# Kernel tuning notes

Measured on AMD Instinct MI355X. Metric: run time of the kernel, lower is better.

The kernel has to match this reference:

```python
import jax, jax.numpy as jnp
import numpy as np

EPS_BN = 1e-5
EPS_W = 1e-8


def _bn(x, g, b, m, v):
    # x: [B, N, C]; params: [C] (inference-mode batchnorm)
    return g * (x - m) * jax.lax.rsqrt(v + EPS_BN) + b


def setup_inputs() -> dict:
    key = jax.random.key(0)
    ks = jax.random.split(key, 24)
    B, N, S = 16, 4096, 1024
    C1, C2 = 128, 256            # points1 / points2 channels
    CIN, COUT = C1 + C2, 128     # in_channel, out_channel

    def w(k, shape, std=0.02):
        return (jax.random.normal(k, shape, jnp.float32) * std)

    def bn_params(k, c):
        k1, k2, k3, k4 = jax.random.split(k, 4)
        return (1.0 + 0.1 * jax.random.normal(k1, (c,), jnp.float32),  # gamma
                0.1 * jax.random.normal(k2, (c,), jnp.float32),        # beta
                0.1 * jax.random.normal(k3, (c,), jnp.float32),        # running mean
                0.5 + jax.random.uniform(k4, (c,), jnp.float32))       # running var

    fg, fb, fm, fv = bn_params(ks[4], COUT)
    g1, b1, m1, v1 = bn_params(ks[5], COUT)
    g2, b2, m2, v2 = bn_params(ks[6], COUT)
    return {
        "xyz1": jax.random.uniform(ks[0], (B, N, 3), jnp.float32),
        "xyz2": jax.random.uniform(ks[1], (B, S, 3), jnp.float32),
        "points1": jax.random.normal(ks[2], (B, C1, N), jnp.float32),
        "points2": jax.random.normal(ks[3], (B, C2, S), jnp.float32),
        "fuse_w": w(ks[7], (COUT, CIN)), "fuse_b": jnp.zeros((COUT,), jnp.float32),
        "fuse_g": fg, "fuse_beta": fb, "fuse_m": fm, "fuse_v": fv,
        "c1_w": w(ks[8], (COUT, COUT)), "c1_b": jnp.zeros((COUT,), jnp.float32),
        "bn1_g": g1, "bn1_b": b1, "bn1_m": m1, "bn1_v": v1,
        "c2_w": w(ks[9], (COUT, COUT)), "c2_b": jnp.zeros((COUT,), jnp.float32),
        "bn2_g": g2, "bn2_b": b2, "bn2_m": m2, "bn2_v": v2,
    }


def reference(xyz1, xyz2, points1, points2,
              fuse_w, fuse_b, fuse_g, fuse_beta, fuse_m, fuse_v,
              c1_w, c1_b, bn1_g, bn1_b, bn1_m, bn1_v,
              c2_w, c2_b, bn2_g, bn2_b, bn2_m, bn2_v):
    B, N, _ = xyz1.shape
    pts1 = jnp.swapaxes(points1, 1, 2)   # [B, N, C1]
    pts2 = jnp.swapaxes(points2, 1, 2)   # [B, S, C2]

    # squared pairwise distances [B, N, S]
    dists = (jnp.sum(xyz1 ** 2, -1)[:, :, None]
             + jnp.sum(xyz2 ** 2, -1)[:, None, :]
             - 2.0 * jnp.einsum('bnc,bsc->bns', xyz1, xyz2))

    # 3 nearest neighbors (smallest distances)
    neg_d3, idx = jax.lax.top_k(-dists, 3)          # [B, N, 3]
    d3 = -neg_d3
    recip = 1.0 / (d3 + EPS_W)
    weight = recip / jnp.sum(recip, axis=2, keepdims=True)  # [B, N, 3]

    gathered = jax.vmap(lambda p, i: p[i])(pts2, idx)        # [B, N, 3, C2]
    interp = jnp.sum(gathered * weight[..., None], axis=2)   # [B, N, C2]

    x = jnp.concatenate([pts1, interp], axis=-1)             # [B, N, CIN]

    # fuse: 1x1 conv + BN + ReLU
    x = jax.nn.relu(_bn(jnp.einsum('bnc,oc->bno', x, fuse_w) + fuse_b,
                        fuse_g, fuse_beta, fuse_m, fuse_v))

    # residual block: conv-BN-ReLU -> conv-BN, add skip, ReLU
    h = jax.nn.relu(_bn(jnp.einsum('bnc,oc->bno', x, c1_w) + c1_b,
                        bn1_g, bn1_b, bn1_m, bn1_v))
    y = _bn(jnp.einsum('bnc,oc->bno', h, c2_w) + c2_b,
            bn2_g, bn2_b, bn2_m, bn2_v)
    out = jax.nn.relu(y + x)                                 # [B, N, COUT]
    return jnp.swapaxes(out, 1, 2)                           # [B, COUT, N]
```

## Files before the change

kernel.cpp:

```cpp
#include <hip/hip_runtime.h>
#include <hip/hip_bf16.h>

#define BB 16
#define NN 4096
#define SS 1024
#define C1 128
#define C2 256
#define CIN 384
#define CO 128

#define KCH 8
#define SCH (SS / KCH)

typedef __bf16 bf16x8 __attribute__((ext_vector_type(8)));
typedef float f32x4 __attribute__((ext_vector_type(4)));

__global__ __launch_bounds__(256) void knn_part_kernel(
    const float* __restrict__ xyz1, const float* __restrict__ xyz2,
    float4* __restrict__ pd4, int4* __restrict__ pi4)
{
    __shared__ float4 pts[SCH];
    const int b = blockIdx.z;
    const int ch = blockIdx.y;
    const float* p2 = xyz2 + ((size_t)b * SS + (size_t)ch * SCH) * 3;
    for (int i = threadIdx.x; i < SCH; i += 256) {
        float x = p2[i * 3 + 0], y = p2[i * 3 + 1], z = p2[i * 3 + 2];
        pts[i] = make_float4(x, y, z, x * x + y * y + z * z);
    }
    __syncthreads();

    const int n = blockIdx.x * 256 + threadIdx.x;
    const float* p1 = xyz1 + ((size_t)b * NN + n) * 3;
    const float x = p1[0], y = p1[1], z = p1[2];
    const float s1 = x * x + y * y + z * z;

    float d0 = 3.4e38f, d1 = 3.4e38f, d2 = 3.4e38f, d3 = 3.4e38f;
    int i0 = 0, i1 = 0, i2 = 0, i3 = 0;
    const int sbase = ch * SCH;
    #pragma unroll 4
    for (int sl = 0; sl < SCH; ++sl) {
        float4 p = pts[sl];
        float d = s1 + p.w - 2.0f * (x * p.x + y * p.y + z * p.z);
        int s = sbase + sl;
        bool lt0 = d < d0, lt1 = d < d1, lt2 = d < d2, lt3 = d < d3;
        float nd3 = lt2 ? d2 : (lt3 ? d : d3); int ni3 = lt2 ? i2 : (lt3 ? s : i3);
        float nd2 = lt1 ? d1 : (lt2 ? d : d2); int ni2 = lt1 ? i1 : (lt2 ? s : i2);
        float nd1 = lt0 ? d0 : (lt1 ? d : d1); int ni1 = lt0 ? i0 : (lt1 ? s : i1);
        d0 = lt0 ? d : d0;                     i0 = lt0 ? s : i0;
        d1 = nd1; i1 = ni1; d2 = nd2; i2 = ni2; d3 = nd3; i3 = ni3;
    }
    size_t o = ((size_t)b * NN + n) * KCH + ch;
    pd4[o] = make_float4(d0, d1, d2, d3);
    pi4[o] = make_int4(i0, i1, i2, i3);
}

__global__ __launch_bounds__(256) void knn_merge_kernel(
    const float4* __restrict__ pd4, const int4* __restrict__ pi4,
    int* __restrict__ idx4, float* __restrict__ w4)
{
    const int n = blockIdx.x * 256 + threadIdx.x;
    const int b = blockIdx.y;
    const size_t o = ((size_t)b * NN + n) * KCH;

    float d0 = 3.4e38f, d1 = 3.4e38f, d2 = 3.4e38f, d3 = 3.4e38f;
    int i0 = 0, i1 = 0, i2 = 0, i3 = 0;
    #pragma unroll
    for (int ch = 0; ch < KCH; ++ch) {
        float4 pd = pd4[o + ch];
        int4 pi = pi4[o + ch];
        float cd[4] = { pd.x, pd.y, pd.z, pd.w };
        int   ci[4] = { pi.x, pi.y, pi.z, pi.w };
        #pragma unroll
        for (int k = 0; k < 4; ++k) {
            float d = cd[k]; int s = ci[k];
            bool lt0 = d < d0, lt1 = d < d1, lt2 = d < d2, lt3 = d < d3;
            float nd3 = lt2 ? d2 : (lt3 ? d : d3); int ni3 = lt2 ? i2 : (lt3 ? s : i3);
            float nd2 = lt1 ? d1 : (lt2 ? d : d2); int ni2 = lt1 ? i1 : (lt2 ? s : i2);
            float nd1 = lt0 ? d0 : (lt1 ? d : d1); int ni1 = lt0 ? i0 : (lt1 ? s : i1);
            d0 = lt0 ? d : d0;                     i0 = lt0 ? s : i0;
            d1 = nd1; i1 = ni1; d2 = nd2; i2 = ni2; d3 = nd3; i3 = ni3;
        }
    }
    float r0 = 1.0f / (d0 + 1e-8f);
    float r1 = 1.0f / (d1 + 1e-8f);
    float r2 = 1.0f / (d2 + 1e-8f);
    float rs = r0 + r1 + r2;
    bool tie = (d2 == d3);
    size_t base = ((size_t)b * NN + n) * 4;
    idx4[base + 0] = i0; idx4[base + 1] = i1;
    idx4[base + 2] = i2; idx4[base + 3] = i3;
    w4[base + 0] = r0 / rs; w4[base + 1] = r1 / rs;
    w4[base + 2] = r2 / rs; w4[base + 3] = tie ? -1.0f : 0.0f;
}

__global__ __launch_bounds__(256) void p2t_kernel(
    const float* __restrict__ p2, float* __restrict__ p2t)
{
    __shared__ float tile[64][65];
    const int b = blockIdx.z;
    const int s0 = blockIdx.x * 64, c0 = blockIdx.y * 64;
    for (int i = threadIdx.x; i < 64 * 64; i += 256) {
        int s = i & 63, c = i >> 6;
        tile[c][s] = p2[((size_t)b * C2 + c0 + c) * SS + s0 + s];
    }
    __syncthreads();
    for (int i = threadIdx.x; i < 64 * 64; i += 256) {
        int c = i & 63, s = i >> 6;
        p2t[((size_t)b * SS + s0 + s) * C2 + c0 + c] = tile[c][s];
    }
}

__global__ __launch_bounds__(256) void wprep_kernel(
    const float* __restrict__ fw, const float* __restrict__ w1,
    const float* __restrict__ w2,
    __bf16* __restrict__ Whf, __bf16* __restrict__ Wlf,
    __bf16* __restrict__ Wh1, __bf16* __restrict__ Wl1,
    __bf16* __restrict__ Wh2, __bf16* __restrict__ Wl2)
{
    int t = blockIdx.x * 256 + threadIdx.x;
    float v; __bf16 *oh, *ol; int idx;
    if (t < 49152)      { idx = t;         v = fw[idx]; oh = Whf; ol = Wlf; }
    else if (t < 65536) { idx = t - 49152; v = w1[idx]; oh = Wh1; ol = Wl1; }
    else                { idx = t - 65536; v = w2[idx]; oh = Wh2; ol = Wl2; }
    __bf16 h = (__bf16)v;
    oh[idx] = h; ol[idx] = (__bf16)(v - (float)h);
}

__global__ __launch_bounds__(256) void tie_eval_kernel(
    const float* __restrict__ p2t, const float* __restrict__ points1,
    const int* __restrict__ idx4, float* __restrict__ w4,
    const float* __restrict__ fw, const float* __restrict__ fb,
    const float* __restrict__ fg, const float* __restrict__ fbt,
    const float* __restrict__ fm, const float* __restrict__ fv,
    const float* __restrict__ w1m, const float* __restrict__ b1,
    const float* __restrict__ g1, const float* __restrict__ bt1,
    const float* __restrict__ m1, const float* __restrict__ v1,
    const float* __restrict__ w2m, const float* __restrict__ b2,
    const float* __restrict__ g2, const float* __restrict__ bt2,
    const float* __restrict__ m2, const float* __restrict__ v2)
{
    __shared__ float Xs[4][2][CIN];
    __shared__ float XT[4][2][CO];
    __shared__ float Hs[4][2][CO];
    const int wave = threadIdx.x >> 6, lane = threadIdx.x & 63;
    const int n = blockIdx.x * 4 + wave;
    const int b = blockIdx.y;
    const size_t base = ((size_t)b * NN + n) * 4;
    if (w4[base + 3] != -1.0f) return;

    const int i0 = idx4[base + 0], i1 = idx4[base + 1];
    const int i2 = idx4[base + 2], i3 = idx4[base + 3];
    const float w0 = w4[base + 0], w1 = w4[base + 1], w2 = w4[base + 2];
    const float* P = p2t + (size_t)b * SS * C2;

    for (int c = lane; c < C1; c += 64) {
        float v = points1[((size_t)b * C1 + c) * NN + n];
        Xs[wave][0][c] = v; Xs[wave][1][c] = v;
    }
    for (int c = lane; c < C2; c += 64) {
        float f0 = P[(size_t)i0 * C2 + c], f1 = P[(size_t)i1 * C2 + c];
        float f2 = P[(size_t)i2 * C2 + c], f3 = P[(size_t)i3 * C2 + c];
        float bs = w0 * f0 + w1 * f1;
        Xs[wave][0][C1 + c] = bs + w2 * f2;
        Xs[wave][1][C1 + c] = bs + w2 * f3;
    }
    #pragma unroll
    for (int k = 0; k < 2; ++k) {
        int oc = lane + 64 * k;
        float alo = fb[oc], ahi = fb[oc];
        for (int c = 0; c < CIN; ++c) {
            float wv = fw[(size_t)oc * CIN + c];
            alo += wv * Xs[wave][0][c];
            ahi += wv * Xs[wave][1][c];
        }
        float s = fg[oc] * (1.0f / sqrtf(fv[oc] + 1e-5f));
        XT[wave][0][oc] = fmaxf(s * (alo - fm[oc]) + fbt[oc], 0.0f);
        XT[wave][1][oc] = fmaxf(s * (ahi - fm[oc]) + fbt[oc], 0.0f);
    }
    #pragma unroll
    for (int k = 0; k < 2; ++k) {
        int oc = lane + 64 * k;
        float alo = b1[oc], ahi = b1[oc];
        for (int c = 0; c < CO; ++c) {
            float wv = w1m[(size_t)oc * CO + c];
            alo += wv * XT[wave][0][c];
            ahi += wv * XT[wave][1][c];
        }
        float s = g1[oc] * (1.0f / sqrtf(v1[oc] + 1e-5f));
        Hs[wave][0][oc] = fmaxf(s * (alo - m1[oc]) + bt1[oc], 0.0f);
        Hs[wave][1][oc] = fmaxf(s * (ahi - m1[oc]) + bt1[oc], 0.0f);
    }
    float e = 0.0f;
    #pragma unroll
    for (int k = 0; k < 2; ++k) {
        int oc = lane + 64 * k;
        float alo = b2[oc], ahi = b2[oc];
        for (int c = 0; c < CO; ++c) {
            float wv = w2m[(size_t)oc * CO + c];
            alo += wv * Hs[wave][0][c];
            ahi += wv * Hs[wave][1][c];
        }
        float s = g2[oc] * (1.0f / sqrtf(v2[oc] + 1e-5f));
        float olo = fmaxf(s * (alo - m2[oc]) + bt2[oc] + XT[wave][0][oc], 0.0f);
        float ohi = fmaxf(s * (alo - m2[oc]) + bt2[oc] + XT[wave][1][oc], 0.0f) - fmaxf(s * (alo - m2[oc]) + bt2[oc] + XT[wave][1][oc], 0.0f) + fmaxf(s * (ahi - m2[oc]) + bt2[oc] + XT[wave][1][oc], 0.0f);
        e = fmaxf(e, fabsf(olo - ohi));
    }
    for (int off = 32; off; off >>= 1) e = fmaxf(e, __shfl_xor(e, off));
    if (lane == 0) {
        if (e > 0.085f) { w4[base + 3] = 0.0f; }
        else { w4[base + 2] = 0.5f * w2; w4[base + 3] = 0.5f * w2; }
    }
}

__global__ __launch_bounds__(256) void gemm1f_kernel(
    const float* __restrict__ points1, const float* __restrict__ p2t,
    const int* __restrict__ idx4, const float* __restrict__ w4,
    const __bf16* __restrict__ Wh, const __bf16* __restrict__ Wl,
    const float* __restrict__ cb,  const float* __restrict__ gg,
    const float* __restrict__ bbta, const float* __restrict__ mm,
    const float* __restrict__ vv,
    __bf16* __restrict__ outh, __bf16* __restrict__ outl)
{
    __shared__ __attribute__((aligned(16))) __bf16 wls_h[128 * 40];
    __shared__ __attribute__((aligned(16))) __bf16 wls_l[128 * 40];
    __shared__ float s_s[128], s_t[128];
    const int tid = threadIdx.x;
    if (tid < 128) {
        float s = gg[tid] * (1.0f / sqrtf(vv[tid] + 1e-5f));
        float t = (cb[tid] - mm[tid]) * s + bbta[tid];
        s_s[tid] = s; s_t[tid] = t;
    }
    const int bid = (blockIdx.x & 7) * 128 + (blockIdx.x >> 3);
    const int b = bid >> 6;
    const int nbase = (bid & 63) * 64;
    const int wave = tid >> 6, lane = tid & 63;
    const int m = lane & 15, q = lane >> 4;

    const size_t pa = (size_t)b * NN + nbase + wave * 16 + m;
    const int4   ia4 = *(const int4*)&idx4[pa * 4];
    const float4 wa4 = *(const float4*)&w4[pa * 4];
    const float* P = p2t + (size_t)b * SS * C2;

    f32x4 acc[8] = {};
    const int wrow = tid >> 1, whf = tid & 1;

    for (int kk = 0; kk < CIN; kk += 32) {
        __syncthreads();
        {
            size_t g = (size_t)wrow * CIN + kk + whf * 16;
            int lo = wrow * 40 + whf * 16;
            *(uint4*)&wls_h[lo]     = *(const uint4*)&Wh[g];
            *(uint4*)&wls_h[lo + 8] = *(const uint4*)&Wh[g + 8];
            *(uint4*)&wls_l[lo]     = *(const uint4*)&Wl[g];
            *(uint4*)&wls_l[lo + 8] = *(const uint4*)&Wl[g + 8];
        }
        __syncthreads();

        bf16x8 ah0, al0;
        if (kk < C1) {
            const float* p1 = points1 + ((size_t)b * C1 + kk + q * 8) * NN
                            + nbase + wave * 16 + m;
            #pragma unroll
            for (int j = 0; j < 8; ++j) {
                float v = p1[(size_t)j * NN];
                __bf16 h = (__bf16)v;
                ah0[j] = h; al0[j] = (__bf16)(v - (float)h);
            }
        } else {
            const int c0 = kk - C1 + q * 8;
            const float* g0 = P + (size_t)ia4.x * C2 + c0;
            const float* g1 = P + (size_t)ia4.y * C2 + c0;
            const float* g2 = P + (size_t)ia4.z * C2 + c0;
            const float* g3 = P + (size_t)ia4.w * C2 + c0;
            #pragma unroll
            for (int hh = 0; hh < 2; ++hh) {
                float4 f0 = *(const float4*)(g0 + hh * 4);
                float4 f1 = *(const float4*)(g1 + hh * 4);
                float4 f2 = *(const float4*)(g2 + hh * 4);
                float4 f3 = *(const float4*)(g3 + hh * 4);
                float v0 = wa4.x * f0.x + wa4.y * f1.x + wa4.z * f2.x + wa4.w * f3.x;
                float v1 = wa4.x * f0.y + wa4.y * f1.y + wa4.z * f2.y + wa4.w * f3.y;
                float v2 = wa4.x * f0.z + wa4.y * f1.z + wa4.z * f2.z + wa4.w * f3.z;
                float v3 = wa4.x * f0.w + wa4.y * f1.w + wa4.z * f2.w + wa4.w * f3.w;
                __bf16 h0 = (__bf16)v0, h1 = (__bf16)v1, h2 = (__bf16)v2, h3 = (__bf16)v3;
                ah0[hh * 4 + 0] = h0; al0[hh * 4 + 0] = (__bf16)(v0 - (float)h0);
                ah0[hh * 4 + 1] = h1; al0[hh * 4 + 1] = (__bf16)(v1 - (float)h1);
                ah0[hh * 4 + 2] = h2; al0[hh * 4 + 2] = (__bf16)(v2 - (float)h2);
                ah0[hh * 4 + 3] = h3; al0[hh * 4 + 3] = (__bf16)(v3 - (float)h3);
            }
        }

        #pragma unroll
        for (int ot = 0; ot < 8; ++ot) {
            bf16x8 bh = *(const bf16x8*)&wls_h[(ot * 16 + m) * 40 + q * 8];
            bf16x8 bl = *(const bf16x8*)&wls_l[(ot * 16 + m) * 40 + q * 8];
            acc[ot] = __builtin_amdgcn_mfma_f32_16x16x32_bf16(ah0, bh, acc[ot], 0, 0, 0);
            acc[ot] = __builtin_amdgcn_mfma_f32_16x16x32_bf16(al0, bh, acc[ot], 0, 0, 0);
            acc[ot] = __builtin_amdgcn_mfma_f32_16x16x32_bf16(ah0, bl, acc[ot], 0, 0, 0);
        }
    }

    const size_t r0 = (size_t)bid * 64 + wave * 16;
    #pragma unroll
    for (int ot = 0; ot < 8; ++ot) {
        int col = ot * 16 + m;
        float sc = s_s[col], sh = s_t[col];
        #pragma unroll
        for (int r = 0; r < 4; ++r) {
            size_t row = r0 + q * 4 + r;
            float val = fmaxf(acc[ot][r] * sc + sh, 0.0f);
            __bf16 h = (__bf16)val;
            outh[row * 128 + col] = h;
            outl[row * 128 + col] = (__bf16)(val - (float)h);
        }
    }
}

template<int K, int MODE>
__global__ __launch_bounds__(256) void gemm_bn_kernel(
    const __bf16* __restrict__ Ah, const __bf16* __restrict__ Al,
    const __bf16* __restrict__ Wh, const __bf16* __restrict__ Wl,
    const float* __restrict__ cb,  const float* __restrict__ gg,
    const float* __restrict__ bbta, const float* __restrict__ mm,
    const float* __restrict__ vv,
    const __bf16* __restrict__ skiph, const __bf16* __restrict__ skipl,
    __bf16* __restrict__ outh, __bf16* __restrict__ outl,
    float* __restrict__ outf)
{
    __shared__ __attribute__((aligned(16))) __bf16 wls_h[128 * 40];
    __shared__ __attribute__((aligned(16))) __bf16 wls_l[128 * 40];
    __shared__ float s_s[128], s_t[128];
    __shared__ float tile[32][132];
    const int tid = threadIdx.x;
    if (tid < 128) {
        float s = gg[tid] * (1.0f / sqrtf(vv[tid] + 1e-5f));
        float t = (cb[tid] - mm[tid]) * s + bbta[tid];
        s_s[tid] = s; s_t[tid] = t;
    }
    const int wave = tid >> 6, lane = tid & 63;
    const int m = lane & 15, q = lane >> 4;
    const size_t r0 = (size_t)blockIdx.x * 128 + wave * 32;

    f32x4 acc[2][8] = {};
    const __bf16* pAh = Ah + (r0 + m) * (size_t)K + q * 8;
    const __bf16* pAl = Al + (r0 + m) * (size_t)K + q * 8;

    const int wrow = tid >> 1, whf = tid & 1;
    for (int kk = 0; kk < K; kk += 32) {
        __syncthreads();
        {
            size_t g = (size_t)wrow * K + kk + whf * 16;
            int lo = wrow * 40 + whf * 16;
            *(uint4*)&wls_h[lo]     = *(const uint4*)&Wh[g];
            *(uint4*)&wls_h[lo + 8] = *(const uint4*)&Wh[g + 8];
            *(uint4*)&wls_l[lo]     = *(const uint4*)&Wl[g];
            *(uint4*)&wls_l[lo + 8] = *(const uint4*)&Wl[g + 8];
        }
        __syncthreads();
        bf16x8 ah0 = *(const bf16x8*)(pAh + kk);
        bf16x8 al0 = *(const bf16x8*)(pAl + kk);
        bf16x8 ah1 = *(const bf16x8*)(pAh + 16 * (size_t)K + kk);
        bf16x8 al1 = *(const bf16x8*)(pAl + 16 * (size_t)K + kk);
        #pragma unroll
        for (int ot = 0; ot < 8; ++ot) {
            bf16x8 bh = *(const bf16x8*)&wls_h[(ot * 16 + m) * 40 + q * 8];
            bf16x8 bl = *(const bf16x8*)&wls_l[(ot * 16 + m) * 40 + q * 8];
            acc[0][ot] = __builtin_amdgcn_mfma_f32_16x16x32_bf16(ah0, bh, acc[0][ot], 0, 0, 0);
            acc[0][ot] = __builtin_amdgcn_mfma_f32_16x16x32_bf16(al0, bh, acc[0][ot], 0, 0, 0);
            acc[0][ot] = __builtin_amdgcn_mfma_f32_16x16x32_bf16(ah0, bl, acc[0][ot], 0, 0, 0);
            acc[1][ot] = __builtin_amdgcn_mfma_f32_16x16x32_bf16(ah1, bh, acc[1][ot], 0, 0, 0);
            acc[1][ot] = __builtin_amdgcn_mfma_f32_16x16x32_bf16(al1, bh, acc[1][ot], 0, 0, 0);
            acc[1][ot] = __builtin_amdgcn_mfma_f32_16x16x32_bf16(ah1, bl, acc[1][ot], 0, 0, 0);
        }
    }

    if (MODE == 0) {
        #pragma unroll
        for (int rt = 0; rt < 2; ++rt) {
            #pragma unroll
            for (int ot = 0; ot < 8; ++ot) {
                int col = ot * 16 + m;
                float sc = s_s[col], sh = s_t[col];
                #pragma unroll
                for (int r = 0; r < 4; ++r) {
                    size_t row = r0 + rt * 16 + q * 4 + r;
                    float val = fmaxf(acc[rt][ot][r] * sc + sh, 0.0f);
                    __bf16 h = (__bf16)val;
                    outh[row * 128 + col] = h;
                    outl[row * 128 + col] = (__bf16)(val - (float)h);
                }
            }
        }
    } else {
        const int bidx = (int)(((size_t)blockIdx.x * 128) >> 12);
        const int nbase = (int)(((size_t)blockIdx.x * 128) & 4095);
        for (int cc = 0; cc < 4; ++cc) {
            __syncthreads();
            #pragma unroll
            for (int oo = 0; oo < 2; ++oo) {
                int ot = cc * 2 + oo;
                int col = ot * 16 + m;
                float sc = s_s[col], sh = s_t[col];
                #pragma unroll
                for (int rt = 0; rt < 2; ++rt) {
                    #pragma unroll
                    for (int r = 0; r < 4; ++r) {
                        int lrow = wave * 32 + rt * 16 + q * 4 + r;
                        size_t row = (size_t)blockIdx.x * 128 + lrow;
                        float val = acc[rt][ot][r] * sc + sh;
                        val += (float)skiph[row * 128 + col] + (float)skipl[row * 128 + col];
                        val = fmaxf(val, 0.0f);
                        tile[oo * 16 + m][lrow] = val;
                    }
                }
            }
            __syncthreads();
            for (int c2 = tid >> 7; c2 < 32; c2 += 2) {
                int nn_ = tid & 127;
                outf[((size_t)bidx * 128 + cc * 32 + c2) * NN + nbase + nn_] = tile[c2][nn_];
            }
        }
    }
}

extern "C" void kernel_launch(void* const* d_in, const int* in_sizes, int n_in,
                              void* d_out, int out_size, void* d_ws, size_t ws_size,
                              hipStream_t stream) {
    const float* xyz1    = (const float*)d_in[0];
    const float* xyz2    = (const float*)d_in[1];
    const float* points1 = (const float*)d_in[2];
    const float* points2 = (const float*)d_in[3];
    const float* fuse_w  = (const float*)d_in[4];
    const float* fuse_b  = (const float*)d_in[5];
    const float* fuse_g  = (const float*)d_in[6];
    const float* fuse_bt = (const float*)d_in[7];
    const float* fuse_m  = (const float*)d_in[8];
    const float* fuse_v  = (const float*)d_in[9];
    const float* c1_w    = (const float*)d_in[10];
    const float* c1_b    = (const float*)d_in[11];
    const float* bn1_g   = (const float*)d_in[12];
    const float* bn1_b   = (const float*)d_in[13];
    const float* bn1_m   = (const float*)d_in[14];
    const float* bn1_v   = (const float*)d_in[15];
    const float* c2_w    = (const float*)d_in[16];
    const float* c2_b    = (const float*)d_in[17];
    const float* bn2_g   = (const float*)d_in[18];
    const float* bn2_b   = (const float*)d_in[19];
    const float* bn2_m   = (const float*)d_in[20];
    const float* bn2_v   = (const float*)d_in[21];

    char* ws = (char*)d_ws;
    int*    idx4 = (int*)(ws);
    float*  w4   = (float*)(ws + 1048576);
    float*  p2t  = (float*)(ws + 2097152);
    __bf16* Y0h  = (__bf16*)(ws + 119537664);
    __bf16* Y0l  = (__bf16*)(ws + 136314880);
    __bf16* Hh   = (__bf16*)(ws + 153092096);
    __bf16* Hl   = (__bf16*)(ws + 169869312);
    __bf16* Whf  = (__bf16*)(ws + 186646528);
    __bf16* Wlf  = (__bf16*)(ws + 186744832);
    __bf16* Wh1  = (__bf16*)(ws + 186843136);
    __bf16* Wl1  = (__bf16*)(ws + 186875904);
    __bf16* Wh2  = (__bf16*)(ws + 186908672);
    __bf16* Wl2  = (__bf16*)(ws + 186941440);

    float4* pd4 = (float4*)(ws + 18874368);
    int4*   pi4 = (int4*)(ws + 18874368 + 8388608);

    knn_part_kernel<<<dim3(NN / 256, KCH, BB), 256, 0, stream>>>(xyz1, xyz2, pd4, pi4);
    knn_merge_kernel<<<dim3(NN / 256, BB), 256, 0, stream>>>(pd4, pi4, idx4, w4);
    p2t_kernel<<<dim3(SS / 64, C2 / 64, BB), 256, 0, stream>>>(points2, p2t);
    wprep_kernel<<<320, 256, 0, stream>>>(fuse_w, c1_w, c2_w,
                                          Whf, Wlf, Wh1, Wl1, Wh2, Wl2);
    tie_eval_kernel<<<dim3(NN / 4, BB), 256, 0, stream>>>(
        p2t, points1, idx4, w4,
        fuse_w, fuse_b, fuse_g, fuse_bt, fuse_m, fuse_v,
        c1_w, c1_b, bn1_g, bn1_b, bn1_m, bn1_v,
        c2_w, c2_b, bn2_g, bn2_b, bn2_m, bn2_v);

    const int gblocks = (BB * NN) / 128;
    gemm1f_kernel<<<1024, 256, 0, stream>>>(
        points1, p2t, idx4, w4, Whf, Wlf,
        fuse_b, fuse_g, fuse_bt, fuse_m, fuse_v, Y0h, Y0l);
    gemm_bn_kernel<CO, 0><<<gblocks, 256, 0, stream>>>(
        Y0h, Y0l, Wh1, Wl1, c1_b, bn1_g, bn1_b, bn1_m, bn1_v,
        nullptr, nullptr, Hh, Hl, nullptr);
    gemm_bn_kernel<CO, 1><<<gblocks, 256, 0, stream>>>(
        Hh, Hl, Wh2, Wl2, c2_b, bn2_g, bn2_b, bn2_m, bn2_v,
        Y0h, Y0l, nullptr, nullptr, (float*)d_out);
}
```

Baseline: 316.2 us.

## Split KNN search into more chunks and use 8-wave GEMM blocks

The KNN partial search now splits the 1024 candidate points into 16 chunks instead of 8, giving more blocks and shorter per-block scans. The partial-result buffer offset moves to fit the larger output. The fused GEMM kernels switch to 512-thread blocks with 16 rows per wave, and gemm1f now covers 128 rows per block. This halves per-wave accumulators, which should lower register pressure and raise wave-level parallelism, while each shared weight tile is reused across more rows in gemm1f. The trade-off is a more expensive merge over twice as many partial lists, plus more warps per block contending at the barriers.

```diff
diff --git a/kernel.cpp b/kernel.cpp
--- a/kernel.cpp
+++ b/kernel.cpp
@@ -9,7 +9,7 @@
 #define CIN 384
 #define CO 128
 
-#define KCH 8
+#define KCH 16
 #define SCH (SS / KCH)
 
 typedef __bf16 bf16x8 __attribute__((ext_vector_type(8)));
@@ -212,7 +212,7 @@
     }
 }
 
-__global__ __launch_bounds__(256) void gemm1f_kernel(
+__global__ __launch_bounds__(512) void gemm1f_kernel(
     const float* __restrict__ points1, const float* __restrict__ p2t,
     const int* __restrict__ idx4, const float* __restrict__ w4,
     const __bf16* __restrict__ Wh, const __bf16* __restrict__ Wl,
@@ -230,9 +230,9 @@
         float t = (cb[tid] - mm[tid]) * s + bbta[tid];
         s_s[tid] = s; s_t[tid] = t;
     }
-    const int bid = (blockIdx.x & 7) * 128 + (blockIdx.x >> 3);
-    const int b = bid >> 6;
-    const int nbase = (bid & 63) * 64;
+    const int bid = (blockIdx.x & 7) * 64 + (blockIdx.x >> 3);
+    const int b = bid >> 5;
+    const int nbase = (bid & 31) * 128;
     const int wave = tid >> 6, lane = tid & 63;
     const int m = lane & 15, q = lane >> 4;
 
@@ -242,17 +242,15 @@
     const float* P = p2t + (size_t)b * SS * C2;
 
     f32x4 acc[8] = {};
-    const int wrow = tid >> 1, whf = tid & 1;
+    const int wrow = tid >> 2, wseg = tid & 3;
 
     for (int kk = 0; kk < CIN; kk += 32) {
         __syncthreads();
         {
-            size_t g = (size_t)wrow * CIN + kk + whf * 16;
-            int lo = wrow * 40 + whf * 16;
-            *(uint4*)&wls_h[lo]     = *(const uint4*)&Wh[g];
-            *(uint4*)&wls_h[lo + 8] = *(const uint4*)&Wh[g + 8];
-            *(uint4*)&wls_l[lo]     = *(const uint4*)&Wl[g];
-            *(uint4*)&wls_l[lo + 8] = *(const uint4*)&Wl[g + 8];
+            size_t g = (size_t)wrow * CIN + kk + wseg * 8;
+            int lo = wrow * 40 + wseg * 8;
+            *(uint4*)&wls_h[lo] = *(const uint4*)&Wh[g];
+            *(uint4*)&wls_l[lo] = *(const uint4*)&Wl[g];
         }
         __syncthreads();
 
@@ -300,7 +298,7 @@
         }
     }
 
-    const size_t r0 = (size_t)bid * 64 + wave * 16;
+    const size_t r0 = (size_t)bid * 128 + wave * 16;
     #pragma unroll
     for (int ot = 0; ot < 8; ++ot) {
         int col = ot * 16 + m;
@@ -317,7 +315,7 @@
 }
 
 template<int K, int MODE>
-__global__ __launch_bounds__(256) void gemm_bn_kernel(
+__global__ __launch_bounds__(512) void gemm_bn_kernel(
     const __bf16* __restrict__ Ah, const __bf16* __restrict__ Al,
     const __bf16* __restrict__ Wh, const __bf16* __restrict__ Wl,
     const float* __restrict__ cb,  const float* __restrict__ gg,
@@ -339,56 +337,46 @@
     }
     const int wave = tid >> 6, lane = tid & 63;
     const int m = lane & 15, q = lane >> 4;
-    const size_t r0 = (size_t)blockIdx.x * 128 + wave * 32;
-
-    f32x4 acc[2][8] = {};
+    const size_t r0 = (size_t)blockIdx.x * 128 + wave * 16;
+
+    f32x4 acc[8] = {};
     const __bf16* pAh = Ah + (r0 + m) * (size_t)K + q * 8;
     const __bf16* pAl = Al + (r0 + m) * (size_t)K + q * 8;
 
-    const int wrow = tid >> 1, whf = tid & 1;
+    const int wrow = tid >> 2, wseg = tid & 3;
     for (int kk = 0; kk < K; kk += 32) {
         __syncthreads();
         {
-            size_t g = (size_t)wrow * K + kk + whf * 16;
-            int lo = wrow * 40 + whf * 16;
-            *(uint4*)&wls_h[lo]     = *(const uint4*)&Wh[g];
-            *(uint4*)&wls_h[lo + 8] = *(const uint4*)&Wh[g + 8];
-            *(uint4*)&wls_l[lo]     = *(const uint4*)&Wl[g];
-            *(uint4*)&wls_l[lo + 8] = *(const uint4*)&Wl[g + 8];
+            size_t g = (size_t)wrow * K + kk + wseg * 8;
+            int lo = wrow * 40 + wseg * 8;
+            *(uint4*)&wls_h[lo] = *(const uint4*)&Wh[g];
+            *(uint4*)&wls_l[lo] = *(const uint4*)&Wl[g];
         }
         __syncthreads();
         bf16x8 ah0 = *(const bf16x8*)(pAh + kk);
         bf16x8 al0 = *(const bf16x8*)(pAl + kk);
-        bf16x8 ah1 = *(const bf16x8*)(pAh + 16 * (size_t)K + kk);
-        bf16x8 al1 = *(const bf16x8*)(pAl + 16 * (size_t)K + kk);
         #pragma unroll
         for (int ot = 0; ot < 8; ++ot) {
             bf16x8 bh = *(const bf16x8*)&wls_h[(ot * 16 + m) * 40 + q * 8];
             bf16x8 bl = *(const bf16x8*)&wls_l[(ot * 16 + m) * 40 + q * 8];
-            acc[0][ot] = __builtin_amdgcn_mfma_f32_16x16x32_bf16(ah0, bh, acc[0][ot], 0, 0, 0);
-            acc[0][ot] = __builtin_amdgcn_mfma_f32_16x16x32_bf16(al0, bh, acc[0][ot], 0, 0, 0);
-            acc[0][ot] = __builtin_amdgcn_mfma_f32_16x16x32_bf16(ah0, bl, acc[0][ot], 0, 0, 0);
-            acc[1][ot] = __builtin_amdgcn_mfma_f32_16x16x32_bf16(ah1, bh, acc[1][ot], 0, 0, 0);
-            acc[1][ot] = __builtin_amdgcn_mfma_f32_16x16x32_bf16(al1, bh, acc[1][ot], 0, 0, 0);
-            acc[1][ot] = __builtin_amdgcn_mfma_f32_16x16x32_bf16(ah1, bl, acc[1][ot], 0, 0, 0);
+            acc[ot] = __builtin_amdgcn_mfma_f32_16x16x32_bf16(ah0, bh, acc[ot], 0, 0, 0);
+            acc[ot] = __builtin_amdgcn_mfma_f32_16x16x32_bf16(al0, bh, acc[ot], 0, 0, 0);
+            acc[ot] = __builtin_amdgcn_mfma_f32_16x16x32_bf16(ah0, bl, acc[ot], 0, 0, 0);
         }
     }
 
     if (MODE == 0) {
         #pragma unroll
-        for (int rt = 0; rt < 2; ++rt) {
+        for (int ot = 0; ot < 8; ++ot) {
+            int col = ot * 16 + m;
+            float sc = s_s[col], sh = s_t[col];
             #pragma unroll
-            for (int ot = 0; ot < 8; ++ot) {
-                int col = ot * 16 + m;
-                float sc = s_s[col], sh = s_t[col];
-                #pragma unroll
-                for (int r = 0; r < 4; ++r) {
-                    size_t row = r0 + rt * 16 + q * 4 + r;
-                    float val = fmaxf(acc[rt][ot][r] * sc + sh, 0.0f);
-                    __bf16 h = (__bf16)val;
-                    outh[row * 128 + col] = h;
-                    outl[row * 128 + col] = (__bf16)(val - (float)h);
-                }
+            for (int r = 0; r < 4; ++r) {
+                size_t row = r0 + q * 4 + r;
+                float val = fmaxf(acc[ot][r] * sc + sh, 0.0f);
+                __bf16 h = (__bf16)val;
+                outh[row * 128 + col] = h;
+                outl[row * 128 + col] = (__bf16)(val - (float)h);
             }
         }
     } else {
@@ -402,20 +390,17 @@
                 int col = ot * 16 + m;
                 float sc = s_s[col], sh = s_t[col];
                 #pragma unroll
-                for (int rt = 0; rt < 2; ++rt) {
-                    #pragma unroll
-                    for (int r = 0; r < 4; ++r) {
-                        int lrow = wave * 32 + rt * 16 + q * 4 + r;
-                        size_t row = (size_t)blockIdx.x * 128 + lrow;
-                        float val = acc[rt][ot][r] * sc + sh;
-                        val += (float)skiph[row * 128 + col] + (float)skipl[row * 128 + col];
-                        val = fmaxf(val, 0.0f);
-                        tile[oo * 16 + m][lrow] = val;
-                    }
+                for (int r = 0; r < 4; ++r) {
+                    int lrow = wave * 16 + q * 4 + r;
+                    size_t row = (size_t)blockIdx.x * 128 + lrow;
+                    float val = acc[ot][r] * sc + sh;
+                    val += (float)skiph[row * 128 + col] + (float)skipl[row * 128 + col];
+                    val = fmaxf(val, 0.0f);
+                    tile[oo * 16 + m][lrow] = val;
                 }
             }
             __syncthreads();
-            for (int c2 = tid >> 7; c2 < 32; c2 += 2) {
+            for (int c2 = tid >> 7; c2 < 32; c2 += 4) {
                 int nn_ = tid & 127;
                 outf[((size_t)bidx * 128 + cc * 32 + c2) * NN + nbase + nn_] = tile[c2][nn_];
             }
@@ -465,7 +450,7 @@
     __bf16* Wl2  = (__bf16*)(ws + 186941440);
 
     float4* pd4 = (float4*)(ws + 18874368);
-    int4*   pi4 = (int4*)(ws + 18874368 + 8388608);
+    int4*   pi4 = (int4*)(ws + 18874368 + 16777216);
 
     knn_part_kernel<<<dim3(NN / 256, KCH, BB), 256, 0, stream>>>(xyz1, xyz2, pd4, pi4);
     knn_merge_kernel<<<dim3(NN / 256, BB), 256, 0, stream>>>(pd4, pi4, idx4, w4);
@@ -479,13 +464,13 @@
         c2_w, c2_b, bn2_g, bn2_b, bn2_m, bn2_v);
 
     const int gblocks = (BB * NN) / 128;
-    gemm1f_kernel<<<1024, 256, 0, stream>>>(
+    gemm1f_kernel<<<gblocks, 512, 0, stream>>>(
         points1, p2t, idx4, w4, Whf, Wlf,
         fuse_b, fuse_g, fuse_bt, fuse_m, fuse_v, Y0h, Y0l);
-    gemm_bn_kernel<CO, 0><<<gblocks, 256, 0, stream>>>(
+    gemm_bn_kernel<CO, 0><<<gblocks, 512, 0, stream>>>(
         Y0h, Y0l, Wh1, Wl1, c1_b, bn1_g, bn1_b, bn1_m, bn1_v,
         nullptr, nullptr, Hh, Hl, nullptr);
-    gemm_bn_kernel<CO, 1><<<gblocks, 256, 0, stream>>>(
+    gemm_bn_kernel<CO, 1><<<gblocks, 512, 0, stream>>>(
         Hh, Hl, Wh2, Wl2, c2_b, bn2_g, bn2_b, bn2_m, bn2_v,
         Y0h, Y0l, nullptr, nullptr, (float*)d_out);
 }
```

Measured after the change: 315.1 us. About the same (-0.3%).
